# Performance work log

Hardware: AMD Instinct MI355X
Metric: run time of the kernel (lower is better)

Reference implementation:

```python
import jax, jax.numpy as jnp
import numpy as np

B, C, M = 2048, 1, 80  # M = max_object; matrices are (M+1)x(M+1)


def setup_inputs() -> dict:
    key = jax.random.key(0)
    k1, k2, k3, k4 = jax.random.split(key, 4)
    inp = {
        "input": jax.random.normal(k1, (B, C, M + 1, M + 1), dtype=jnp.float32),
        "target": jax.random.randint(k2, (B, C, M + 1, M + 1), 0, 2, dtype=jnp.int32),
        "mask0": jax.random.randint(k3, (B, C, M + 1), 0, 2, dtype=jnp.int32),
        "mask1": jax.random.randint(k4, (B, C, M + 1), 0, 2, dtype=jnp.int32),
        "outputs": 0,
        "current_fair_labels": 0,
        "next_fair_labels": 0,
    }
    return inp


def reference(input, target, mask0, mask1, outputs, current_fair_labels, next_fair_labels):
    f32 = jnp.float32
    m0 = mask0.astype(f32)[:, :, :, None]   # [B,C,M+1,1] (row mask, broadcast over cols)
    m1 = mask1.astype(f32)[:, :, None, :]   # [B,C,1,M+1] (col mask, broadcast over rows)
    mask_region = m0 * m1                    # [B,C,M+1,M+1]
    mask_region_pre = mask_region.at[:, :, M, :].set(0.0)   # zero last row
    mask_region_next = mask_region.at[:, :, :, M].set(0.0)  # zero last col
    mask_region_union = mask_region_pre * mask_region_next

    input_pre = jax.nn.softmax(mask_region_pre * input, axis=3)
    input_next = jax.nn.softmax(mask_region_next * input, axis=2)
    input_all = input_pre.at[:, :, :M, :M].set(
        jnp.maximum(input_pre, input_next)[:, :, :M, :M])

    t = target.astype(jnp.bool_).astype(f32)
    target_pre = mask_region_pre * t
    target_next = mask_region_next * t
    target_union = mask_region_union * t

    target_num = t.sum()
    n_pre = target_pre.sum()
    n_next = target_next.sum()
    n_union = target_union.sum()

    s_pre = -(target_pre * jnp.log(input_pre)).sum()
    loss_pre = jnp.where(n_pre > 0, s_pre / n_pre, s_pre)

    s_next = -(target_next * jnp.log(input_next)).sum()
    loss_next = jnp.where(n_next > 0, s_next / n_next, s_next)

    s_all = -(target_pre * jnp.log(input_all)).sum()
    loss = jnp.where((n_pre > 0) & (n_next > 0), s_all / n_pre, s_all)

    # |1 - p_pre - (1 - p_next)| == |p_next - p_pre|
    s_sim = (target_union * jnp.abs(input_next - input_pre)).sum()
    loss_similarity = jnp.where(n_union > 0, s_sim / target_num, s_sim)

    # accuracy on "pre" direction (argmax over cols, drop last row)
    idx_t_pre = jnp.argmax(target_pre, axis=3)[:, :, :-1]
    indexes_pre = jnp.argmax(input_all, axis=3)[:, :, :-1]
    mpre = mask0.astype(f32)[:, :, :-1]
    n_mpre = mpre.sum()
    s_acc_pre = ((indexes_pre == idx_t_pre).astype(f32) * mpre).sum()
    accuracy_pre = jnp.where(n_mpre > 0, s_acc_pre / n_mpre, s_acc_pre + 1.0)

    # accuracy on "next" direction (argmax over rows, drop last col)
    idx_t_next = jnp.argmax(target_next, axis=2)[:, :, :-1]
    indexes_next = jnp.argmax(input_next, axis=2)[:, :, :-1]
    mnext = mask1.astype(f32)[:, :, :-1]
    n_mnext = mnext.sum()
    s_acc_next = ((indexes_next == idx_t_next).astype(f32) * mnext).sum()
    accuracy_next = jnp.where(n_mnext > 0, s_acc_next / n_mnext, s_acc_next + 1.0)

    total = (loss_pre + loss_next + loss + loss_similarity) / 4.0
    return (loss_pre, loss_next, loss_similarity, total,
            accuracy_pre, accuracy_next, (accuracy_pre + accuracy_next) / 2.0,
            indexes_pre)
```

## Files before the change

### kernel.cpp

```cpp
#include <hip/hip_runtime.h>

#define M1 81
#define MSZ 80
#define NEL (M1 * M1)
#define NTW ((NEL + 31) / 32)
#define NACC 12
#define BIGKC 1.0e30f
#define REDP 517


__global__ __launch_bounds__(512, 8) void sst_main(
    const float* __restrict__ input,
    const int* __restrict__ target,
    const int* __restrict__ mask0,
    const int* __restrict__ mask1,
    float* __restrict__ out_idx,
    float* __restrict__ part,
    int slices)
{
    __shared__ __align__(16) float s_x[NEL];
    __shared__ unsigned s_tb[NTW];
    __shared__ float s_m0[M1], s_m1[M1];
    __shared__ float s_kc[M1];
    __shared__ float s_invc[M1];
    __shared__ unsigned char s_ci[M1];
    __shared__ int s_ct[MSZ];
    __shared__ unsigned s_m1w[4];

    const int tid   = threadIdx.x;
    const int lane  = tid & 63;
    const int slice = blockIdx.x;
    const size_t base = (size_t)slice * NEL;

    const bool act = (tid < 4 * M1);
    const int g   = tid >> 2;
    const int j4  = tid & 3;
    const int c0j = (j4 == 0) ? 0 : (1 + 20 * j4);
    const int lm1 = (j4 == 0) ? 0x1FFFFF : 0xFFFFF;

    if (tid < M1) s_m0[tid] = (float)mask0[slice * M1 + tid];
    else if (tid >= 128 && tid < 128 + M1) s_m1[tid - 128] = (float)mask1[slice * M1 + (tid - 128)];
    if (tid >= 256 && tid < 256 + MSZ) s_ct[tid - 256] = 0x7fffffff;

    float a[NACC];
#pragma unroll
    for (int k = 0; k < NACC; ++k) a[k] = 0.0f;

    __syncthreads();

    float v[21];
    if (act) {
        const float* gp = input + base + (size_t)c0j * M1 + g;
#pragma unroll
        for (int i = 0; i < 20; ++i) v[i] = gp[i * M1];
        v[20] = gp[((j4 == 0) ? 20 : 0) * M1];
    }

    int tpre[13];
#pragma unroll
    for (int k = 0; k < 13; ++k) {
        const int i = tid + (k << 9);
        tpre[k] = (i < NEL) ? target[base + i] : 0;
    }

    if ((tid >> 6) == 0) {
        const unsigned long long m = __ballot(s_m1[lane] != 0.0f);
        if (lane == 0) { s_m1w[0] = (unsigned)m; s_m1w[1] = (unsigned)(m >> 32); }
    } else if ((tid >> 6) == 1) {
        float vv = 0.0f;
        if (lane < 17) vv = s_m1[64 + lane];
        const unsigned long long m = __ballot(vv != 0.0f);
        if (lane == 0) { s_m1w[2] = (unsigned)m; s_m1w[3] = 0u; }
    }

    if (act) {
        const int c = g;
        const float m1c = s_m1[c];
        float cs = 0.0f, bv = -1.0f;
        int bi = c0j;
        int idx = c0j * M1 + c;
#pragma unroll
        for (int i = 0; i < 20; ++i, idx += M1) {
            const int r = c0j + i;
            const float z = m1c * s_m0[r] * v[i];
            const float e = __expf(z);
            s_x[idx] = e;
            cs += e;
            if (e > bv) { bv = e; bi = r; }
        }
        if (j4 == 0) {
            const float z = m1c * s_m0[20] * v[20];
            const float e = __expf(z);
            s_x[20 * M1 + c] = e;
            cs += e;
            if (e > bv) { bv = e; bi = 20; }
        }
#pragma unroll
        for (int m = 1; m <= 2; m <<= 1) {
            const float pcs = __shfl_xor(cs, m);
            const float pbv = __shfl_xor(bv, m);
            const int   pbi = __shfl_xor(bi, m);
            cs += pcs;
            const bool take = (lane & m) ? (pbv >= bv) : (pbv > bv);
            if (take) { bv = pbv; bi = pbi; }
        }
        if (j4 == 0) {
            s_kc[c]   = (c == MSZ) ? BIGKC : __logf(cs);
            s_invc[c] = (c == MSZ) ? 0.0f  : 1.0f / cs;
            s_ci[c]   = (unsigned char)bi;
        }
    }

#pragma unroll
    for (int k = 0; k < 13; ++k) {
        const int i = tid + (k << 9);
        if (i < NEL) {
            const unsigned long long m = __ballot(tpre[k] != 0);
            if (lane == 0) {
                a[0] += (float)__popcll(m);
                const int w2 = (i >> 5) & ~1;
                s_tb[w2] = (unsigned)m;
                if (w2 + 1 < NTW) s_tb[w2 + 1] = (unsigned)(m >> 32);
            }
        }
    }
    __syncthreads();

    if (act) {
        const int r = g;
        const int rb = r * M1;
        const int bp = rb + c0j;
        const unsigned long long tw64 =
            ((unsigned long long)s_tb[(bp >> 5) + 1] << 32) | s_tb[bp >> 5];
        const int mp0 = c0j >> 5;
        const unsigned long long mw64 =
            ((unsigned long long)s_m1w[mp0 + 1] << 32) | s_m1w[mp0];
        unsigned wb = (unsigned)(tw64 >> (bp & 31)) & (unsigned)(mw64 >> (c0j & 31)) & (unsigned)lm1;

        if (r < MSZ) {
            const float m0f = s_m0[r];
            if (m0f == 0.0f) wb = 0u;
            float rs = 0.0f;
#pragma unroll
            for (int i = 0; i < 20; ++i) rs += s_x[rb + c0j + i];
            if (j4 == 0) rs += s_x[rb + 20];
            rs += __shfl_xor(rs, 1);
            rs += __shfl_xor(rs, 2);
            const float lr = __logf(rs), invr = 1.0f / rs;

            const unsigned w3 = (j4 == 3) ? (wb & 0x7FFFFu) : wb;
            a[1] += (float)__popc(wb);
            a[2] += (float)__popc(w3);
            a[3] += (float)__popc(w3);
            int ti = wb ? (c0j + __ffs(wb) - 1) : 127;

            float bv = -1.0f; int bi = c0j;
#pragma unroll
            for (int i = 0; i < 20; ++i) {
                const int c = c0j + i;
                const float val = s_x[rb + c] * fmaxf(invr, s_invc[c]);
                if (val > bv) { bv = val; bi = c; }
            }
            if (j4 == 0) {
                const float val = s_x[rb + 20] * fmaxf(invr, s_invc[20]);
                if (val > bv) { bv = val; bi = 20; }
            }
            unsigned wl = wb;
            while (wl) {
                const int b = __ffs(wl) - 1; wl &= wl - 1u;
                const int c = c0j + b;
                const float e = s_x[rb + c];
                const float z = __logf(e);
                a[4] += lr - z;
                a[6] += fminf(lr, s_kc[c]) - z;
                if (c != MSZ) {
                    a[5] += s_kc[c] - z;
                    a[7] = fmaf(e, fabsf(s_invc[c] - invr), a[7]);
                    atomicMin(&s_ct[c], r);
                }
            }
#pragma unroll
            for (int m = 1; m <= 2; m <<= 1) {
                const float pbv = __shfl_xor(bv, m);
                const int   pbi = __shfl_xor(bi, m);
                const int   pti = __shfl_xor(ti, m);
                const bool take = (lane & m) ? (pbv >= bv) : (pbv > bv);
                if (take) { bv = pbv; bi = pbi; }
                ti = min(ti, pti);
            }
            if (j4 == 0) {
                if (ti == 127) ti = 0;
                out_idx[(size_t)slice * MSZ + r] = (float)bi;
                a[8]  += (bi == ti) ? m0f : 0.0f;
                a[10] += m0f;
            }
        } else {
            if (s_m0[MSZ] == 0.0f) wb = 0u;
            if (j4 == 3) wb &= 0x7FFFFu;
            a[2] += (float)__popc(wb);
            while (wb) {
                const int b = __ffs(wb) - 1; wb &= wb - 1u;
                const int c = c0j + b;
                a[5] += s_kc[c] - __logf(s_x[rb + c]);
                atomicMin(&s_ct[c], MSZ);
            }
        }
    }
    __syncthreads();

    if (tid < MSZ) {
        const int ctv = s_ct[tid];
        const int ti = (ctv == 0x7fffffff) ? 0 : ctv;
        const int bi = (int)s_ci[tid];
        const float m1c = s_m1[tid];
        a[9]  += (bi == ti) ? m1c : 0.0f;
        a[11] += m1c;
    }

    float* red = s_x;
#pragma unroll
    for (int k = 0; k < NACC; ++k) red[k * REDP + tid] = a[k];
    __syncthreads();
    if (tid < 96) {
        const int k = tid >> 3, u = tid & 7;
        const int b0 = k * REDP + u * 64;
        const int i0 = u * 4;
        float s = 0.0f;
        for (int i = 0; i < 64; ++i) s += red[b0 + ((i0 + i) & 63)];
        s += __shfl_xor(s, 1);
        s += __shfl_xor(s, 2);
        s += __shfl_xor(s, 4);
        if (u == 0) part[(size_t)k * slices + slice] = s;
    }
}

__global__ __launch_bounds__(256) void sst_final(
    const float* __restrict__ part, int slices, float* __restrict__ out)
{
    __shared__ double s_part[4][NACC];
    const int tid = threadIdx.x;
    double l[NACC];
#pragma unroll
    for (int k = 0; k < NACC; ++k) l[k] = 0.0;
    for (int s = tid; s < slices; s += 256) {
#pragma unroll
        for (int k = 0; k < NACC; ++k) l[k] += (double)part[(size_t)k * slices + s];
    }
#pragma unroll
    for (int k = 0; k < NACC; ++k) {
        double v = l[k];
        for (int off = 32; off > 0; off >>= 1) v += __shfl_down(v, off);
        if ((tid & 63) == 0) s_part[tid >> 6][k] = v;
    }
    __syncthreads();
    if (tid == 0) {
        double g[NACC];
#pragma unroll
        for (int k = 0; k < NACC; ++k)
            g[k] = s_part[0][k] + s_part[1][k] + s_part[2][k] + s_part[3][k];
        const double tnum = g[0], npre = g[1], nnext = g[2], nunion = g[3];
        const double spre = g[4], snext = g[5], sall = g[6], ssim = g[7];
        const double accp = g[8], accn = g[9], nmp = g[10], nmn = g[11];
        const double loss_pre  = (npre > 0.0) ? spre / npre : spre;
        const double loss_next = (nnext > 0.0) ? snext / nnext : snext;
        const double loss      = (npre > 0.0 && nnext > 0.0) ? sall / npre : sall;
        const double loss_sim  = (nunion > 0.0) ? ssim / tnum : ssim;
        const double total = (loss_pre + loss_next + loss + loss_sim) * 0.25;
        const double ap = (nmp > 0.0) ? accp / nmp : accp + 1.0;
        const double an = (nmn > 0.0) ? accn / nmn : accn + 1.0;
        out[0] = (float)loss_pre;
        out[1] = (float)loss_next;
        out[2] = (float)loss_sim;
        out[3] = (float)total;
        out[4] = (float)ap;
        out[5] = (float)an;
        out[6] = (float)((ap + an) * 0.5);
    }
}

extern "C" void kernel_launch(void* const* d_in, const int* in_sizes, int n_in,
                              void* d_out, int out_size, void* d_ws, size_t ws_size,
                              hipStream_t stream) {
    const float* input  = (const float*)d_in[0];
    const int*   target = (const int*)d_in[1];
    const int*   mask0  = (const int*)d_in[2];
    const int*   mask1  = (const int*)d_in[3];
    float* out = (float*)d_out;
    float* part = (float*)d_ws;

    const int slices = in_sizes[0] / NEL;

    sst_main<<<slices, 512, 0, stream>>>(input, target, mask0, mask1, out + 7, part, slices);
    sst_final<<<1, 256, 0, stream>>>(part, slices, out);
}
```

Before: 151.7 us.

## Process two slices per block, prefetching second slice during first

Each block now handles two consecutive slices. While the first slice's row sweep runs, the second slice's input values and masks are already being loaded, so global-memory latency is overlapped with compute. This halves the block count and the partial-sum count the final reduction reads, at the cost of serialising two slices inside one block, adding barriers, and extra register pressure from keeping prefetched values live.

```diff
diff --git a/kernel.cpp b/kernel.cpp
--- a/kernel.cpp
+++ b/kernel.cpp
@@ -16,21 +16,23 @@
     const int* __restrict__ mask1,
     float* __restrict__ out_idx,
     float* __restrict__ part,
-    int slices)
+    int slices,
+    int nparts)
 {
     __shared__ __align__(16) float s_x[NEL];
     __shared__ unsigned s_tb[NTW];
-    __shared__ float s_m0[M1], s_m1[M1];
+    __shared__ float s_m0[2][M1], s_m1[2][M1];
     __shared__ float s_kc[M1];
     __shared__ float s_invc[M1];
-    __shared__ unsigned char s_ci[M1];
-    __shared__ int s_ct[MSZ];
-    __shared__ unsigned s_m1w[4];
+    __shared__ unsigned char s_ci[2][M1];
+    __shared__ int s_ct[2][MSZ];
+    __shared__ unsigned s_m1w[2][4];
 
     const int tid   = threadIdx.x;
     const int lane  = tid & 63;
-    const int slice = blockIdx.x;
-    const size_t base = (size_t)slice * NEL;
+    const int slice0 = blockIdx.x * 2;
+    const int slice1 = slice0 + 1;
+    const bool s2 = (slice1 < slices);
 
     const bool act = (tid < 4 * M1);
     const int g   = tid >> 2;
@@ -38,95 +40,89 @@
     const int c0j = (j4 == 0) ? 0 : (1 + 20 * j4);
     const int lm1 = (j4 == 0) ? 0x1FFFFF : 0xFFFFF;
 
-    if (tid < M1) s_m0[tid] = (float)mask0[slice * M1 + tid];
-    else if (tid >= 128 && tid < 128 + M1) s_m1[tid - 128] = (float)mask1[slice * M1 + (tid - 128)];
-    if (tid >= 256 && tid < 256 + MSZ) s_ct[tid - 256] = 0x7fffffff;
+    if (tid < M1) s_m0[0][tid] = (float)mask0[slice0 * M1 + tid];
+    else if (tid >= 128 && tid < 128 + M1) s_m1[0][tid - 128] = (float)mask1[slice0 * M1 + (tid - 128)];
+    if (tid >= 256 && tid < 256 + MSZ) s_ct[0][tid - 256] = 0x7fffffff;
+    else if (tid >= 352 && tid < 352 + MSZ) s_ct[1][tid - 352] = 0x7fffffff;
 
     float a[NACC];
 #pragma unroll
     for (int k = 0; k < NACC; ++k) a[k] = 0.0f;
 
-    __syncthreads();
-
     float v[21];
-    if (act) {
-        const float* gp = input + base + (size_t)c0j * M1 + g;
-#pragma unroll
-        for (int i = 0; i < 20; ++i) v[i] = gp[i * M1];
-        v[20] = gp[((j4 == 0) ? 20 : 0) * M1];
-    }
-
     int tpre[13];
-#pragma unroll
-    for (int k = 0; k < 13; ++k) {
-        const int i = tid + (k << 9);
-        tpre[k] = (i < NEL) ? target[base + i] : 0;
-    }
-
-    if ((tid >> 6) == 0) {
-        const unsigned long long m = __ballot(s_m1[lane] != 0.0f);
-        if (lane == 0) { s_m1w[0] = (unsigned)m; s_m1w[1] = (unsigned)(m >> 32); }
-    } else if ((tid >> 6) == 1) {
-        float vv = 0.0f;
-        if (lane < 17) vv = s_m1[64 + lane];
-        const unsigned long long m = __ballot(vv != 0.0f);
-        if (lane == 0) { s_m1w[2] = (unsigned)m; s_m1w[3] = 0u; }
-    }
-
-    if (act) {
-        const int c = g;
-        const float m1c = s_m1[c];
-        float cs = 0.0f, bv = -1.0f;
-        int bi = c0j;
-        int idx = c0j * M1 + c;
-#pragma unroll
-        for (int i = 0; i < 20; ++i, idx += M1) {
-            const int r = c0j + i;
-            const float z = m1c * s_m0[r] * v[i];
-            const float e = __expf(z);
-            s_x[idx] = e;
-            cs += e;
-            if (e > bv) { bv = e; bi = r; }
-        }
-        if (j4 == 0) {
-            const float z = m1c * s_m0[20] * v[20];
-            const float e = __expf(z);
-            s_x[20 * M1 + c] = e;
-            cs += e;
-            if (e > bv) { bv = e; bi = 20; }
-        }
-#pragma unroll
-        for (int m = 1; m <= 2; m <<= 1) {
-            const float pcs = __shfl_xor(cs, m);
-            const float pbv = __shfl_xor(bv, m);
-            const int   pbi = __shfl_xor(bi, m);
-            cs += pcs;
-            const bool take = (lane & m) ? (pbv >= bv) : (pbv > bv);
-            if (take) { bv = pbv; bi = pbi; }
-        }
-        if (j4 == 0) {
-            s_kc[c]   = (c == MSZ) ? BIGKC : __logf(cs);
-            s_invc[c] = (c == MSZ) ? 0.0f  : 1.0f / cs;
-            s_ci[c]   = (unsigned char)bi;
-        }
-    }
-
-#pragma unroll
-    for (int k = 0; k < 13; ++k) {
-        const int i = tid + (k << 9);
-        if (i < NEL) {
-            const unsigned long long m = __ballot(tpre[k] != 0);
-            if (lane == 0) {
-                a[0] += (float)__popcll(m);
-                const int w2 = (i >> 5) & ~1;
-                s_tb[w2] = (unsigned)m;
-                if (w2 + 1 < NTW) s_tb[w2 + 1] = (unsigned)(m >> 32);
-            }
-        }
-    }
-    __syncthreads();
-
-    if (act) {
+
+    auto loadV = [&](int sl) {
+        if (act) {
+            const float* gp = input + (size_t)sl * NEL + (size_t)c0j * M1 + g;
+#pragma unroll
+            for (int i = 0; i < 20; ++i) v[i] = gp[i * M1];
+            v[20] = gp[((j4 == 0) ? 20 : 0) * M1];
+        }
+    };
+    auto loadT = [&](int sl) {
+        const size_t tb_ = (size_t)sl * NEL;
+#pragma unroll
+        for (int k = 0; k < 13; ++k) {
+            const int i = tid + (k << 9);
+            tpre[k] = (i < NEL) ? target[tb_ + i] : 0;
+        }
+    };
+    auto bitpack = [&]() {
+#pragma unroll
+        for (int k = 0; k < 13; ++k) {
+            const int i = tid + (k << 9);
+            if (i < NEL) {
+                const unsigned long long m = __ballot(tpre[k] != 0);
+                if (lane == 0) {
+                    a[0] += (float)__popcll(m);
+                    const int w2 = (i >> 5) & ~1;
+                    s_tb[w2] = (unsigned)m;
+                    if (w2 + 1 < NTW) s_tb[w2 + 1] = (unsigned)(m >> 32);
+                }
+            }
+        }
+    };
+    auto sweepA = [&](int p) {
+        if (act) {
+            const int c = g;
+            const float m1c = s_m1[p][c];
+            float cs = 0.0f, bv = -1.0f;
+            int bi = c0j;
+            int idx = c0j * M1 + c;
+#pragma unroll
+            for (int i = 0; i < 20; ++i, idx += M1) {
+                const int r = c0j + i;
+                const float z = m1c * s_m0[p][r] * v[i];
+                const float e = __expf(z);
+                s_x[idx] = e;
+                cs += e;
+                if (e > bv) { bv = e; bi = r; }
+            }
+            if (j4 == 0) {
+                const float z = m1c * s_m0[p][20] * v[20];
+                const float e = __expf(z);
+                s_x[20 * M1 + c] = e;
+                cs += e;
+                if (e > bv) { bv = e; bi = 20; }
+            }
+#pragma unroll
+            for (int m = 1; m <= 2; m <<= 1) {
+                const float pcs = __shfl_xor(cs, m);
+                const float pbv = __shfl_xor(bv, m);
+                const int   pbi = __shfl_xor(bi, m);
+                cs += pcs;
+                const bool take = (lane & m) ? (pbv >= bv) : (pbv > bv);
+                if (take) { bv = pbv; bi = pbi; }
+            }
+            if (j4 == 0) {
+                s_kc[c]   = (c == MSZ) ? BIGKC : __logf(cs);
+                s_invc[c] = (c == MSZ) ? 0.0f  : 1.0f / cs;
+                s_ci[p][c] = (unsigned char)bi;
+            }
+        }
+    };
+    auto sweepC = [&](int p, int sl) {
         const int r = g;
         const int rb = r * M1;
         const int bp = rb + c0j;
@@ -134,11 +130,11 @@
             ((unsigned long long)s_tb[(bp >> 5) + 1] << 32) | s_tb[bp >> 5];
         const int mp0 = c0j >> 5;
         const unsigned long long mw64 =
-            ((unsigned long long)s_m1w[mp0 + 1] << 32) | s_m1w[mp0];
+            ((unsigned long long)s_m1w[p][mp0 + 1] << 32) | s_m1w[p][mp0];
         unsigned wb = (unsigned)(tw64 >> (bp & 31)) & (unsigned)(mw64 >> (c0j & 31)) & (unsigned)lm1;
 
         if (r < MSZ) {
-            const float m0f = s_m0[r];
+            const float m0f = s_m0[p][r];
             if (m0f == 0.0f) wb = 0u;
             float rs = 0.0f;
 #pragma unroll
@@ -176,7 +172,7 @@
                 if (c != MSZ) {
                     a[5] += s_kc[c] - z;
                     a[7] = fmaf(e, fabsf(s_invc[c] - invr), a[7]);
-                    atomicMin(&s_ct[c], r);
+                    atomicMin(&s_ct[p][c], r);
                 }
             }
 #pragma unroll
@@ -190,32 +186,74 @@
             }
             if (j4 == 0) {
                 if (ti == 127) ti = 0;
-                out_idx[(size_t)slice * MSZ + r] = (float)bi;
+                out_idx[(size_t)sl * MSZ + r] = (float)bi;
                 a[8]  += (bi == ti) ? m0f : 0.0f;
                 a[10] += m0f;
             }
         } else {
-            if (s_m0[MSZ] == 0.0f) wb = 0u;
+            if (s_m0[p][MSZ] == 0.0f) wb = 0u;
             if (j4 == 3) wb &= 0x7FFFFu;
             a[2] += (float)__popc(wb);
             while (wb) {
                 const int b = __ffs(wb) - 1; wb &= wb - 1u;
                 const int c = c0j + b;
                 a[5] += s_kc[c] - __logf(s_x[rb + c]);
-                atomicMin(&s_ct[c], MSZ);
-            }
-        }
-    }
-    __syncthreads();
-
-    if (tid < MSZ) {
-        const int ctv = s_ct[tid];
-        const int ti = (ctv == 0x7fffffff) ? 0 : ctv;
-        const int bi = (int)s_ci[tid];
-        const float m1c = s_m1[tid];
-        a[9]  += (bi == ti) ? m1c : 0.0f;
-        a[11] += m1c;
-    }
+                atomicMin(&s_ct[p][c], MSZ);
+            }
+        }
+    };
+    auto accN = [&](int p) {
+        if (tid < MSZ) {
+            const int ctv = s_ct[p][tid];
+            const int ti = (ctv == 0x7fffffff) ? 0 : ctv;
+            const int bi = (int)s_ci[p][tid];
+            const float m1c = s_m1[p][tid];
+            a[9]  += (bi == ti) ? m1c : 0.0f;
+            a[11] += m1c;
+        }
+    };
+
+    __syncthreads();
+
+    loadV(slice0);
+    loadT(slice0);
+    if ((tid >> 6) == 0) {
+        const unsigned long long m = __ballot(s_m1[0][lane] != 0.0f);
+        if (lane == 0) { s_m1w[0][0] = (unsigned)m; s_m1w[0][1] = (unsigned)(m >> 32); }
+    } else if ((tid >> 6) == 1) {
+        float vv = 0.0f;
+        if (lane < 17) vv = s_m1[0][64 + lane];
+        const unsigned long long m = __ballot(vv != 0.0f);
+        if (lane == 0) { s_m1w[0][2] = (unsigned)m; s_m1w[0][3] = 0u; }
+    }
+    sweepA(0);
+    bitpack();
+    __syncthreads();
+
+    if (s2) loadV(slice1);
+    if (act) {
+        sweepC(0, slice0);
+    } else if (tid >= 384 && s2) {
+        const int u = tid - 384;
+        if (u < M1) s_m0[1][u] = (float)mask0[slice1 * M1 + u];
+        float m1v = 0.0f;
+        if (u < M1) { m1v = (float)mask1[slice1 * M1 + u]; s_m1[1][u] = m1v; }
+        const unsigned long long mm = __ballot(m1v != 0.0f);
+        if (u == 0)       { s_m1w[1][0] = (unsigned)mm; s_m1w[1][1] = (unsigned)(mm >> 32); }
+        else if (u == 64) { s_m1w[1][2] = (unsigned)mm; s_m1w[1][3] = 0u; }
+    }
+    __syncthreads();
+
+    accN(0);
+    if (s2) {
+        loadT(slice1);
+        sweepA(1);
+        bitpack();
+    }
+    __syncthreads();
+    if (s2 && act) sweepC(1, slice1);
+    __syncthreads();
+    if (s2) accN(1);
 
     float* red = s_x;
 #pragma unroll
@@ -230,21 +268,21 @@
         s += __shfl_xor(s, 1);
         s += __shfl_xor(s, 2);
         s += __shfl_xor(s, 4);
-        if (u == 0) part[(size_t)k * slices + slice] = s;
+        if (u == 0) part[(size_t)k * nparts + blockIdx.x] = s;
     }
 }
 
 __global__ __launch_bounds__(256) void sst_final(
-    const float* __restrict__ part, int slices, float* __restrict__ out)
+    const float* __restrict__ part, int n, float* __restrict__ out)
 {
     __shared__ double s_part[4][NACC];
     const int tid = threadIdx.x;
     double l[NACC];
 #pragma unroll
     for (int k = 0; k < NACC; ++k) l[k] = 0.0;
-    for (int s = tid; s < slices; s += 256) {
-#pragma unroll
-        for (int k = 0; k < NACC; ++k) l[k] += (double)part[(size_t)k * slices + s];
+    for (int s = tid; s < n; s += 256) {
+#pragma unroll
+        for (int k = 0; k < NACC; ++k) l[k] += (double)part[(size_t)k * n + s];
     }
 #pragma unroll
     for (int k = 0; k < NACC; ++k) {
@@ -288,8 +326,10 @@
     float* out = (float*)d_out;
     float* part = (float*)d_ws;
 
-    const int slices = in_sizes[0] / NEL;
-
-    sst_main<<<slices, 512, 0, stream>>>(input, target, mask0, mask1, out + 7, part, slices);
-    sst_final<<<1, 256, 0, stream>>>(part, slices, out);
+    const int slices  = in_sizes[0] / NEL;
+    const int nblocks = (slices + 1) / 2;
+
+    sst_main<<<nblocks, 512, 0, stream>>>(input, target, mask0, mask1,
+                                          out + 7, part, slices, nblocks);
+    sst_final<<<1, 256, 0, stream>>>(part, nblocks, out);
 }
```

Measured after the change: 159.8 us. 1.05x slower.
